# Kernel optimization log

Hardware: AMD Instinct MI355X
Metric: run time of the kernel (lower is better)

Reference implementation:

```python
import jax, jax.numpy as jnp
import numpy as np

FACTOR = -1.0  # RecurrentAdditiveCell(units=11, factor=-1)


def setup_inputs() -> dict:
    key = jax.random.key(0)
    B, S, F = 1024, 4096, 11
    x = jax.random.normal(key, (B, S, F), dtype=jnp.float32)
    initial_state = jnp.zeros((B, 1), dtype=jnp.float32)
    return {"x": x, "initial_state": initial_state}


def reference(x, initial_state):
    # Cell: state_t = state_{t-1} + FACTOR * x_t, unrolled over time.
    # Equivalent closed form: init (broadcast over feat) + FACTOR * cumsum(x, time).
    # return_sequences=True -> emit every step's state: [B, S, F]
    y = initial_state[:, None, :] + FACTOR * jnp.cumsum(x, axis=1)
    return y
```

## Files before the change

kernel.cpp:

```cpp
#include <hip/hip_runtime.h>

#define BATCH    1024
#define SEQ      4096
#define FEAT     11
#define FACTOR   (-1.0f)

#define NTHREADS 256
#define TS       1024
#define NT       (SEQ / TS)
#define CPT      (TS / NTHREADS)
#define FPT      (CPT * FEAT)
#define TILE_FLOATS (TS * FEAT)
#define TILE_F4  (TILE_FLOATS / 4)
#define VL       (TILE_F4 / NTHREADS)

__global__ __launch_bounds__(NTHREADS)
void rnn_scan_kernel(const float* __restrict__ x,
                     const float* __restrict__ init_state,
                     float* __restrict__ y) {
    __shared__ float4 tile_lds[TILE_F4];
    __shared__ float  waveTot[4][FEAT];

    const int b    = blockIdx.x;
    const int t    = threadIdx.x;
    const int lane = t & 63;
    const int wav  = t >> 6;

    const float4* __restrict__ xg =
        (const float4*)(x + (size_t)b * (SEQ * FEAT));
    float4* __restrict__ yg =
        (float4*)(y + (size_t)b * (SEQ * FEAT));
    const float init_v = init_state[b];

    float carry[FEAT];
#pragma unroll
    for (int f = 0; f < FEAT; ++f) carry[f] = 0.0f;

    float4 cur[VL];
#pragma unroll
    for (int i = 0; i < VL; ++i) cur[i] = xg[t + NTHREADS * i];

#pragma unroll
    for (int tile = 0; tile < NT; ++tile) {
#pragma unroll
        for (int i = 0; i < VL; ++i) tile_lds[t + NTHREADS * i] = cur[i];
        __syncthreads();

        if (tile + 1 < NT) {
#pragma unroll
            for (int i = 0; i < VL; ++i)
                cur[i] = xg[(tile + 1) * TILE_F4 + t + NTHREADS * i];
        }

        float v[FPT];
#pragma unroll
        for (int k = 0; k < VL; ++k) {
            float4 q = tile_lds[VL * t + k];
            v[4 * k + 0] = q.x; v[4 * k + 1] = q.y;
            v[4 * k + 2] = q.z; v[4 * k + 3] = q.w;
        }
#pragma unroll
        for (int s = 1; s < CPT; ++s)
#pragma unroll
            for (int f = 0; f < FEAT; ++f)
                v[s * FEAT + f] += v[(s - 1) * FEAT + f];

        float inc[FEAT];
#pragma unroll
        for (int f = 0; f < FEAT; ++f) inc[f] = v[(CPT - 1) * FEAT + f];
#pragma unroll
        for (int d = 1; d < 64; d <<= 1) {
#pragma unroll
            for (int f = 0; f < FEAT; ++f) {
                float o = __shfl_up(inc[f], d, 64);
                if (lane >= d) inc[f] += o;
            }
        }
        if (lane == 63) {
#pragma unroll
            for (int f = 0; f < FEAT; ++f) waveTot[wav][f] = inc[f];
        }
        __syncthreads();

        float base[FEAT];
#pragma unroll
        for (int f = 0; f < FEAT; ++f) {
            float off = carry[f] + inc[f] - v[(CPT - 1) * FEAT + f];
#pragma unroll
            for (int w = 0; w < 4; ++w) {
                float wt = waveTot[w][f];
                if (w < wav) off += wt;
                carry[f] += wt;
            }
            base[f] = off;
        }
#pragma unroll
        for (int s = 0; s < CPT; ++s)
#pragma unroll
            for (int f = 0; f < FEAT; ++f)
                v[s * FEAT + f] = init_v + FACTOR * (base[f] + v[s * FEAT + f]);
#pragma unroll
        for (int k = 0; k < VL; ++k) {
            float4 q;
            q.x = v[4 * k + 0]; q.y = v[4 * k + 1];
            q.z = v[4 * k + 2]; q.w = v[4 * k + 3];
            tile_lds[VL * t + k] = q;
        }
        __syncthreads();

#pragma unroll
        for (int i = 0; i < VL; ++i)
            yg[tile * TILE_F4 + t + NTHREADS * i] = tile_lds[t + NTHREADS * i];
    }
}

extern "C" void kernel_launch(void* const* d_in, const int* in_sizes, int n_in,
                              void* d_out, int out_size, void* d_ws, size_t ws_size,
                              hipStream_t stream) {
    const float* x    = (const float*)d_in[0];
    const float* init = (const float*)d_in[1];
    float*       y    = (float*)d_out;
    rnn_scan_kernel<<<dim3(BATCH), dim3(NTHREADS), 0, stream>>>(x, init, y);
}
```

Before: 344.2 us.

## Load tiles directly per thread, drop LDS staging, use DPP wave scan

Each thread now loads its own 11 contiguous float4 chunks straight from global memory and writes results back the same way, removing the LDS transpose and two barriers per tile. The wave-level prefix sum uses DPP row shifts and row broadcasts instead of shfl_up loops. The wave totals are kept per tile so one barrier per tile is enough, and launch bounds request 4 blocks per CU. The cost is that global accesses become strided per thread (176-byte stride) rather than fully coalesced, and software prefetch of the next tile is removed.

```diff
diff --git a/kernel.cpp b/kernel.cpp
--- a/kernel.cpp
+++ b/kernel.cpp
@@ -1,4 +1,5 @@
 #include <hip/hip_runtime.h>
+
 
 #define BATCH    1024
 #define SEQ      4096
@@ -9,17 +10,30 @@
 #define TS       1024
 #define NT       (SEQ / TS)
 #define CPT      (TS / NTHREADS)
-#define FPT      (CPT * FEAT)
-#define TILE_FLOATS (TS * FEAT)
-#define TILE_F4  (TILE_FLOATS / 4)
-#define VL       (TILE_F4 / NTHREADS)
+#define TILE_F4  (TS * FEAT / 4)
+#define NWAVE    (NTHREADS / 64)
 
-__global__ __launch_bounds__(NTHREADS)
+template <int CTRL, int RM, int BM, bool BC>
+__device__ __forceinline__ float dpp_src(float v) {
+    int r = __builtin_amdgcn_update_dpp(0, __float_as_int(v), CTRL, RM, BM, BC);
+    return __int_as_float(r);
+}
+
+__device__ __forceinline__ float wave_iscan(float x) {
+    x += dpp_src<0x111, 0xf, 0xf, true >(x);
+    x += dpp_src<0x112, 0xf, 0xf, true >(x);
+    x += dpp_src<0x114, 0xf, 0xf, true >(x);
+    x += dpp_src<0x118, 0xf, 0xf, true >(x);
+    x += dpp_src<0x142, 0xa, 0xf, false>(x);
+    x += dpp_src<0x143, 0xc, 0xf, false>(x);
+    return x;
+}
+
+__global__ __launch_bounds__(NTHREADS, 4)
 void rnn_scan_kernel(const float* __restrict__ x,
                      const float* __restrict__ init_state,
                      float* __restrict__ y) {
-    __shared__ float4 tile_lds[TILE_F4];
-    __shared__ float  waveTot[4][FEAT];
+    __shared__ float waveTot[NT][NWAVE][FEAT];
 
     const int b    = blockIdx.x;
     const int t    = threadIdx.x;
@@ -36,29 +50,21 @@
 #pragma unroll
     for (int f = 0; f < FEAT; ++f) carry[f] = 0.0f;
 
-    float4 cur[VL];
-#pragma unroll
-    for (int i = 0; i < VL; ++i) cur[i] = xg[t + NTHREADS * i];
-
 #pragma unroll
     for (int tile = 0; tile < NT; ++tile) {
+        const int base = tile * TILE_F4 + FEAT * t;
+
+        float4 q[FEAT];
 #pragma unroll
-        for (int i = 0; i < VL; ++i) tile_lds[t + NTHREADS * i] = cur[i];
-        __syncthreads();
+        for (int k = 0; k < FEAT; ++k) q[k] = xg[base + k];
 
-        if (tile + 1 < NT) {
+        float v[CPT * FEAT];
 #pragma unroll
-            for (int i = 0; i < VL; ++i)
-                cur[i] = xg[(tile + 1) * TILE_F4 + t + NTHREADS * i];
+        for (int k = 0; k < FEAT; ++k) {
+            v[4 * k + 0] = q[k].x; v[4 * k + 1] = q[k].y;
+            v[4 * k + 2] = q[k].z; v[4 * k + 3] = q[k].w;
         }
 
-        float v[FPT];
-#pragma unroll
-        for (int k = 0; k < VL; ++k) {
-            float4 q = tile_lds[VL * t + k];
-            v[4 * k + 0] = q.x; v[4 * k + 1] = q.y;
-            v[4 * k + 2] = q.z; v[4 * k + 3] = q.w;
-        }
 #pragma unroll
         for (int s = 1; s < CPT; ++s)
 #pragma unroll
@@ -67,50 +73,36 @@
 
         float inc[FEAT];
 #pragma unroll
-        for (int f = 0; f < FEAT; ++f) inc[f] = v[(CPT - 1) * FEAT + f];
-#pragma unroll
-        for (int d = 1; d < 64; d <<= 1) {
-#pragma unroll
-            for (int f = 0; f < FEAT; ++f) {
-                float o = __shfl_up(inc[f], d, 64);
-                if (lane >= d) inc[f] += o;
-            }
-        }
+        for (int f = 0; f < FEAT; ++f)
+            inc[f] = wave_iscan(v[(CPT - 1) * FEAT + f]);
+
         if (lane == 63) {
 #pragma unroll
-            for (int f = 0; f < FEAT; ++f) waveTot[wav][f] = inc[f];
+            for (int f = 0; f < FEAT; ++f) waveTot[tile][wav][f] = inc[f];
         }
         __syncthreads();
 
-        float base[FEAT];
 #pragma unroll
         for (int f = 0; f < FEAT; ++f) {
             float off = carry[f] + inc[f] - v[(CPT - 1) * FEAT + f];
 #pragma unroll
-            for (int w = 0; w < 4; ++w) {
-                float wt = waveTot[w][f];
+            for (int w = 0; w < NWAVE; ++w) {
+                float wt = waveTot[tile][w][f];
                 if (w < wav) off += wt;
                 carry[f] += wt;
             }
-            base[f] = off;
+#pragma unroll
+            for (int s = 0; s < CPT; ++s)
+                v[s * FEAT + f] = init_v + FACTOR * (off + v[s * FEAT + f]);
         }
-#pragma unroll
-        for (int s = 0; s < CPT; ++s)
-#pragma unroll
-            for (int f = 0; f < FEAT; ++f)
-                v[s * FEAT + f] = init_v + FACTOR * (base[f] + v[s * FEAT + f]);
-#pragma unroll
-        for (int k = 0; k < VL; ++k) {
-            float4 q;
-            q.x = v[4 * k + 0]; q.y = v[4 * k + 1];
-            q.z = v[4 * k + 2]; q.w = v[4 * k + 3];
-            tile_lds[VL * t + k] = q;
-        }
-        __syncthreads();
 
 #pragma unroll
-        for (int i = 0; i < VL; ++i)
-            yg[tile * TILE_F4 + t + NTHREADS * i] = tile_lds[t + NTHREADS * i];
+        for (int k = 0; k < FEAT; ++k) {
+            float4 o;
+            o.x = v[4 * k + 0]; o.y = v[4 * k + 1];
+            o.z = v[4 * k + 2]; o.w = v[4 * k + 3];
+            yg[base + k] = o;
+        }
     }
 }
 
```

Result: slower. 378.7 us (+10.0%).
